# Optimization experiments

Hardware: AMD Instinct MI355X
Metric: run time of the kernel (lower is better)

The kernel has to match this reference:

```python
import jax, jax.numpy as jnp
import numpy as np

D = 1024
LEAF_DIM = 512
DEPTH = 3
NUM_LEAVES = 2 ** DEPTH          # 8
NUM_NODES = NUM_LEAVES - 1       # 7
B, T = 4, 2048


def setup_inputs() -> dict:
    key = jax.random.key(0)
    ks = jax.random.split(key, 9)
    sD = 1.0 / np.sqrt(D)
    sH = 1.0 / np.sqrt(LEAF_DIM)
    return {
        "x": jax.random.normal(ks[0], (B, T, D), dtype=jnp.float32),
        "node_kernel": jax.random.normal(ks[1], (D, NUM_NODES), dtype=jnp.float32) * sD,
        "node_bias": jnp.zeros((NUM_NODES,), dtype=jnp.float32),
        "w1a": jax.random.normal(ks[2], (NUM_LEAVES, D, LEAF_DIM), dtype=jnp.float32) * sD,
        "w1b": jax.random.normal(ks[3], (NUM_LEAVES, D, LEAF_DIM), dtype=jnp.float32) * sD,
        "b1a": jnp.zeros((NUM_LEAVES, LEAF_DIM), dtype=jnp.float32),
        "b1b": jnp.zeros((NUM_LEAVES, LEAF_DIM), dtype=jnp.float32),
        "w2": jax.random.normal(ks[4], (NUM_LEAVES, LEAF_DIM, D), dtype=jnp.float32) * sH,
        "b2": jnp.zeros((NUM_LEAVES, D), dtype=jnp.float32),
    }


def reference(x, node_kernel, node_bias, w1a, w1b, b1a, b1b, w2, b2):
    Bx, Tx, Dx = x.shape
    L = NUM_LEAVES
    # hierarchical sigmoid gates over tree nodes: (B,T,num_nodes)
    c = jax.nn.sigmoid(jnp.einsum("btd,dn->btn", x, node_kernel) + node_bias)
    # interleave [c_i, 1-c_i] -> (B,T,2*num_nodes,1), matching original stack+reshape
    c_nc = jnp.stack([c, 1.0 - c], axis=-1).reshape(Bx, Tx, -1)[..., None]
    # build per-leaf mixture weights by descending the tree (depth is a small constant)
    mixture = jnp.ones((Bx, Tx, L), dtype=x.dtype)
    for d in range(DEPTH):
        n2 = 2 ** (d + 1)  # 2 * n_nodes at this level
        mixture = mixture.reshape(Bx, Tx, n2, L // n2) * c_nc[..., :n2, :]
    mixture = mixture.reshape(Bx, Tx, L)
    # per-leaf GLU MLP, batched over the leaf axis
    h = (jnp.einsum("btd,ldh->btlh", x, w1a) + b1a) * (
        jnp.einsum("btd,ldh->btlh", x, w1b) + b1b
    )  # (B,T,L,leaf_dim)
    y = jnp.einsum("btlh,lhd->btld", h, w2) + b2  # (B,T,L,D)
    # weighted combine over leaves
    return (y * mixture[..., None]).sum(axis=-2)  # (B,T,D)
```

## Files before the change

kernel.cpp:

```cpp
#include <hip/hip_runtime.h>


typedef unsigned short u16;
typedef __attribute__((ext_vector_type(8))) short bf16x8;
typedef __attribute__((ext_vector_type(8))) unsigned short u16x8;
typedef __attribute__((ext_vector_type(4))) float f32x4;

__device__ __forceinline__ u16 f2bf(float f) {
  unsigned int u = __builtin_bit_cast(unsigned int, f);
  u += 0x7FFFu + ((u >> 16) & 1u);
  return (u16)(u >> 16);
}

__device__ __forceinline__ void gload16(const void* g, void* l) {
  __builtin_amdgcn_global_load_lds(
      (const __attribute__((address_space(1))) unsigned int*)g,
      (__attribute__((address_space(3))) unsigned int*)l, 16, 0, 0);
}

__device__ __forceinline__ f32x4 MFMA(bf16x8 a, bf16x8 b, f32x4 c) {
  return __builtin_amdgcn_mfma_f32_16x16x32_bf16(a, b, c, 0, 0, 0);
}

#define BARX()                              \
  do {                                      \
    __builtin_amdgcn_sched_barrier(0);      \
    __builtin_amdgcn_s_barrier();           \
    __builtin_amdgcn_sched_barrier(0);      \
  } while (0)

#define VMC(n)                                             \
  do {                                                     \
    __builtin_amdgcn_sched_barrier(0);                     \
    asm volatile("s_waitcnt vmcnt(" #n ")" ::: "memory");  \
    __builtin_amdgcn_sched_barrier(0);                     \
  } while (0)

__global__ void k_gate(const float* __restrict__ x, const float* __restrict__ nk,
                       const float* __restrict__ nb, float* __restrict__ mix) {
  int token = blockIdx.x * 4 + (threadIdx.x >> 6);
  int lane = threadIdx.x & 63;
  const float* xr = x + (size_t)token * 1024;
  float a0 = 0.f, a1 = 0.f, a2 = 0.f, a3 = 0.f;
#pragma unroll
  for (int j = 0; j < 16; ++j) {
    int d = lane + j * 64;
    float xv = xr[d];
    const float* nkd = nk + d * 7;
    a0 = fmaf(xv, nkd[0], a0);
    a1 = fmaf(xv, nkd[1], a1);
    a2 = fmaf(xv, nkd[2], a2);
    a3 = fmaf(xv, nkd[3], a3);
  }
#pragma unroll
  for (int off = 32; off >= 1; off >>= 1) {
    a0 += __shfl_xor(a0, off);
    a1 += __shfl_xor(a1, off);
    a2 += __shfl_xor(a2, off);
    a3 += __shfl_xor(a3, off);
  }
  if (lane == 0) {
    float v[4] = {a0 + nb[0], a1 + nb[1], a2 + nb[2], a3 + nb[3]};
    float cn[8];
#pragma unroll
    for (int i = 0; i < 4; ++i) {
      float s = 1.f / (1.f + expf(-v[i]));
      cn[2 * i] = s;
      cn[2 * i + 1] = 1.f - s;
    }
    float* mr = mix + (size_t)token * 8;
#pragma unroll
    for (int l = 0; l < 8; ++l) mr[l] = cn[l >> 2] * cn[l >> 1] * cn[l];
  }
}

__global__ void k_cast_x(const float* __restrict__ x, u16* __restrict__ xb) {
  size_t i = (size_t)blockIdx.x * blockDim.x + threadIdx.x;
  const float4* p = (const float4*)x + i * 2;
  float4 v0 = p[0], v1 = p[1];
  u16x8 o;
  o[0] = f2bf(v0.x); o[1] = f2bf(v0.y); o[2] = f2bf(v0.z); o[3] = f2bf(v0.w);
  o[4] = f2bf(v1.x); o[5] = f2bf(v1.y); o[6] = f2bf(v1.z); o[7] = f2bf(v1.w);
  *((u16x8*)xb + i) = o;
}

__global__ void k_transpose_cast(const float* __restrict__ in, u16* __restrict__ out,
                                 int R, int C, long out_rstride, long leaf_base) {
  __shared__ float tile[32][33];
  int l = blockIdx.z;
  int c0 = blockIdx.x * 32, r0 = blockIdx.y * 32;
  const float* inl = in + (size_t)l * R * C;
  int tc = threadIdx.x & 31, tr = threadIdx.x >> 5;
#pragma unroll
  for (int i = 0; i < 4; ++i) {
    int r = tr + i * 8;
    tile[r][tc] = inl[(size_t)(r0 + r) * C + c0 + tc];
  }
  __syncthreads();
  u16* outl = out + (size_t)l * leaf_base;
#pragma unroll
  for (int i = 0; i < 4; ++i) {
    int c = tr + i * 8;
    outl[(size_t)(c0 + c) * out_rstride + r0 + tc] = f2bf(tile[tc][c]);
  }
}

__global__ __launch_bounds__(256, 2) void k_glu_gemm(
    const u16* __restrict__ Xb, const u16* __restrict__ Wa, const u16* __restrict__ Wb,
    const float* __restrict__ b1a, const float* __restrict__ b1b,
    const float* __restrict__ mix, u16* __restrict__ H) {
  constexpr int K = 1024, NT = 32;
  __shared__ alignas(16) u16 smem[24576];
  const int tid = threadIdx.x;
  const int logical = (blockIdx.x & 7) * 256 + (blockIdx.x >> 3);
  const int bn = logical >> 6, bm = logical & 63;
  const int m0 = bm * 128, n0 = bn * 128;
  const int wid = tid >> 6, lane = tid & 63;
  const int wm = (wid >> 1) * 64, wn = (wid & 1) * 64;
  const int fr = lane & 15, fk = lane >> 4;

  const int c0_ = tid, c1_ = tid + 256;
  const int r0_ = c0_ >> 2, s0_ = ((c0_ & 3) ^ ((r0_ >> 1) & 3)) * 8;
  const int r1_ = c1_ >> 2, s1_ = ((c1_ & 3) ^ ((r1_ >> 1) & 3)) * 8;

#define STG1(v)                                                                     \
  do {                                                                              \
    const int kb = (v) * 32;                                                        \
    u16* dA = smem + ((v) & 1) * 4096;                                              \
    u16* dBa = smem + 8192 + ((v) & 1) * 4096;                                      \
    u16* dBb = smem + 16384 + ((v) & 1) * 4096;                                     \
    gload16(&Xb[(size_t)(m0 + r0_) * K + kb + s0_], &dA[c0_ * 8]);                  \
    gload16(&Xb[(size_t)(m0 + r1_) * K + kb + s1_], &dA[c1_ * 8]);                  \
    gload16(&Wa[(size_t)(n0 + r0_) * K + kb + s0_], &dBa[c0_ * 8]);                 \
    gload16(&Wa[(size_t)(n0 + r1_) * K + kb + s1_], &dBa[c1_ * 8]);                 \
    gload16(&Wb[(size_t)(n0 + r0_) * K + kb + s0_], &dBb[c0_ * 8]);                 \
    gload16(&Wb[(size_t)(n0 + r1_) * K + kb + s1_], &dBb[c1_ * 8]);                 \
  } while (0)

  f32x4 accA[4][4], accB[4][4];
#pragma unroll
  for (int i = 0; i < 4; ++i)
#pragma unroll
    for (int j = 0; j < 4; ++j) {
      accA[i][j] = (f32x4)0.0f;
      accB[i][j] = (f32x4)0.0f;
    }

  const int slot_ = (fk ^ ((fr >> 1) & 3)) * 8;

  STG1(0);
  VMC(0);
  BARX();
  for (int u = 0; u < NT; ++u) {
    if (u + 1 < NT) STG1(u + 1);
    __builtin_amdgcn_sched_barrier(0);
    const u16* A_ = smem + (u & 1) * 4096;
    const u16* Ba_ = smem + 8192 + (u & 1) * 4096;
    const u16* Bb_ = smem + 16384 + (u & 1) * 4096;
    bf16x8 a_[4], ba_[4], bb_[4];
#pragma unroll
    for (int i = 0; i < 4; ++i) {
      a_[i]  = *(const bf16x8*)&A_[(wm + i * 16 + fr) * 32 + slot_];
      ba_[i] = *(const bf16x8*)&Ba_[(wn + i * 16 + fr) * 32 + slot_];
      bb_[i] = *(const bf16x8*)&Bb_[(wn + i * 16 + fr) * 32 + slot_];
    }
    __builtin_amdgcn_s_setprio(1);
#pragma unroll
    for (int i = 0; i < 4; ++i)
#pragma unroll
      for (int j = 0; j < 4; ++j) {
        accA[i][j] = MFMA(a_[i], ba_[j], accA[i][j]);
        accB[i][j] = MFMA(a_[i], bb_[j], accB[i][j]);
      }
    __builtin_amdgcn_s_setprio(0);
    VMC(0);
    BARX();
  }
#undef STG1

  const int leaf = n0 >> 9;
  const float* b1al = b1a + (leaf << 9);
  const float* b1bl = b1b + (leaf << 9);
  u16* hs = smem;
#pragma unroll
  for (int mf = 0; mf < 4; ++mf)
#pragma unroll
    for (int r = 0; r < 4; ++r) {
      int row_l = wm + mf * 16 + fk * 4 + r;
      float mv = mix[(size_t)(m0 + row_l) * 8 + leaf];
#pragma unroll
      for (int nf = 0; nf < 4; ++nf) {
        int col_l = wn + nf * 16 + fr;
        int hc = (n0 + col_l) & 511;
        float va = accA[mf][nf][r] + b1al[hc];
        float vb = accB[mf][nf][r] + b1bl[hc];
        hs[row_l * 128 + col_l] = f2bf(va * vb * mv);
      }
    }
  BARX();
#pragma unroll
  for (int j = 0; j < 8; ++j) {
    int idx = j * 256 + tid;
    int row_l = idx >> 4;
    int cc = (idx & 15) * 8;
    *(u16x8*)&H[(size_t)(m0 + row_l) * 4096 + n0 + cc] =
        *(const u16x8*)&hs[row_l * 128 + cc];
  }
}

__global__ __launch_bounds__(256, 4) void k_gemm2s(
    const u16* __restrict__ Hm, const u16* __restrict__ W2T,
    const float* __restrict__ b2, const float* __restrict__ mix,
    float* __restrict__ out, float* __restrict__ P1) {
  constexpr int K = 4096, KH = 2048, NT = KH / 32;
  __shared__ alignas(16) u16 smem[16384];
  const int tid = threadIdx.x;
  const int logical = (blockIdx.x & 7) * 128 + (blockIdx.x >> 3);
  const int xcd_chunk = logical >> 7;
  const int i_ = logical & 127;
  const int kc = i_ >> 6;
  const int bn = i_ & 7;
  const int bm = xcd_chunk * 8 + ((i_ >> 3) & 7);
  const int m0 = bm * 128, n0 = bn * 128;
  const size_t kbase = (size_t)kc * KH;
  const int wid = tid >> 6, lane = tid & 63;
  const int wm = (wid >> 1) * 64, wn = (wid & 1) * 64;
  const int fr = lane & 15, fk = lane >> 4;

  const int c0_ = tid, c1_ = tid + 256;
  const int r0_ = c0_ >> 2, s0_ = ((c0_ & 3) ^ ((r0_ >> 1) & 3)) * 8;
  const int r1_ = c1_ >> 2, s1_ = ((c1_ & 3) ^ ((r1_ >> 1) & 3)) * 8;

#define STG2(v)                                                                       \
  do {                                                                                \
    const int kb = (v) * 32;                                                          \
    u16* dA = smem + ((v) & 1) * 4096;                                                \
    u16* dB = smem + 8192 + ((v) & 1) * 4096;                                         \
    gload16(&Hm[(size_t)(m0 + r0_) * K + kbase + kb + s0_], &dA[c0_ * 8]);            \
    gload16(&Hm[(size_t)(m0 + r1_) * K + kbase + kb + s1_], &dA[c1_ * 8]);            \
    gload16(&W2T[(size_t)(n0 + r0_) * K + kbase + kb + s0_], &dB[c0_ * 8]);           \
    gload16(&W2T[(size_t)(n0 + r1_) * K + kbase + kb + s1_], &dB[c1_ * 8]);           \
  } while (0)

  f32x4 acc[4][4];
#pragma unroll
  for (int i = 0; i < 4; ++i)
#pragma unroll
    for (int j = 0; j < 4; ++j) acc[i][j] = (f32x4)0.0f;

  const int slot_ = (fk ^ ((fr >> 1) & 3)) * 8;

  STG2(0);
  VMC(0);
  BARX();
  for (int u = 0; u < NT; ++u) {
    if (u + 1 < NT) STG2(u + 1);
    __builtin_amdgcn_sched_barrier(0);
    const u16* A_ = smem + (u & 1) * 4096;
    const u16* B_ = smem + 8192 + (u & 1) * 4096;
    bf16x8 a_[4], b_[4];
#pragma unroll
    for (int i = 0; i < 4; ++i) {
      a_[i] = *(const bf16x8*)&A_[(wm + i * 16 + fr) * 32 + slot_];
      b_[i] = *(const bf16x8*)&B_[(wn + i * 16 + fr) * 32 + slot_];
    }
    __builtin_amdgcn_s_setprio(1);
#pragma unroll
    for (int i = 0; i < 4; ++i)
#pragma unroll
      for (int j = 0; j < 4; ++j)
        acc[i][j] = MFMA(a_[i], b_[j], acc[i][j]);
    __builtin_amdgcn_s_setprio(0);
    VMC(0);
    BARX();
  }
#undef STG2

  float* dst = (kc == 0) ? out : P1;
  float* os = (float*)smem;
  const int myhalf = wid >> 1;
#pragma unroll
  for (int half = 0; half < 2; ++half) {
    BARX();
    if (myhalf == half) {
#pragma unroll
      for (int nf = 0; nf < 4; ++nf) {
        int col_l = wn + nf * 16 + fr;
        float bc[8];
        if (kc == 0) {
#pragma unroll
          for (int l = 0; l < 8; ++l) bc[l] = b2[l * 1024 + n0 + col_l];
        }
#pragma unroll
        for (int mf = 0; mf < 4; ++mf)
#pragma unroll
          for (int r = 0; r < 4; ++r) {
            int row_lh = mf * 16 + fk * 4 + r;
            float v = acc[mf][nf][r];
            if (kc == 0) {
              const float* mr = mix + (size_t)(m0 + half * 64 + row_lh) * 8;
              float bias = 0.f;
#pragma unroll
              for (int l = 0; l < 8; ++l) bias = fmaf(mr[l], bc[l], bias);
              v += bias;
            }
            os[row_lh * 128 + col_l] = v;
          }
      }
    }
    BARX();
#pragma unroll
    for (int j = 0; j < 8; ++j) {
      int idx = j * 256 + tid;
      int row_lh = idx >> 5;
      int cc = (idx & 31) * 4;
      *(float4*)&dst[(size_t)(m0 + half * 64 + row_lh) * 1024 + n0 + cc] =
          *(const float4*)&os[row_lh * 128 + cc];
    }
  }
}

__global__ void k_add(float* __restrict__ out, const float* __restrict__ P1) {
  size_t i = (size_t)blockIdx.x * 256 + threadIdx.x;
  float4 a = ((const float4*)out)[i];
  float4 b = ((const float4*)P1)[i];
  a.x += b.x; a.y += b.y; a.z += b.z; a.w += b.w;
  ((float4*)out)[i] = a;
}

extern "C" void kernel_launch(void* const* d_in, const int* in_sizes, int n_in,
                              void* d_out, int out_size, void* d_ws, size_t ws_size,
                              hipStream_t stream) {
  const float* x   = (const float*)d_in[0];
  const float* nk  = (const float*)d_in[1];
  const float* nb  = (const float*)d_in[2];
  const float* w1a = (const float*)d_in[3];
  const float* w1b = (const float*)d_in[4];
  const float* b1a = (const float*)d_in[5];
  const float* b1b = (const float*)d_in[6];
  const float* w2  = (const float*)d_in[7];
  const float* b2  = (const float*)d_in[8];
  float* out = (float*)d_out;

  char* ws = (char*)d_ws;
  float* mix = (float*)ws;
  u16* Xb  = (u16*)(ws + 262144);
  u16* WaT = (u16*)(ws + 262144 + 16777216);
  u16* WbT = (u16*)(ws + 262144 + 16777216 + 8388608);
  u16* W2T = (u16*)(ws + 262144 + 16777216 + 2 * 8388608);
  u16* Hs  = (u16*)(ws + 262144 + 16777216 + 3 * 8388608);
  float* P1 = (float*)(ws + 262144);

  k_gate<<<2048, 256, 0, stream>>>(x, nk, nb, mix);
  k_cast_x<<<4096, 256, 0, stream>>>(x, Xb);
  k_transpose_cast<<<dim3(16, 32, 8), 256, 0, stream>>>(w1a, WaT, 1024, 512, 1024L, 512L * 1024L);
  k_transpose_cast<<<dim3(16, 32, 8), 256, 0, stream>>>(w1b, WbT, 1024, 512, 1024L, 512L * 1024L);
  k_transpose_cast<<<dim3(32, 16, 8), 256, 0, stream>>>(w2, W2T, 512, 1024, 4096L, 512L);
  k_glu_gemm<<<2048, 256, 0, stream>>>(Xb, WaT, WbT, b1a, b1b, mix, Hs);
  k_gemm2s<<<1024, 256, 0, stream>>>(Hs, W2T, b2, mix, out, P1);
  k_add<<<8192, 256, 0, stream>>>(out, P1);
}
```

Baseline: 285.4 us.

## Fuse gate with x cast, merge w1 transposes, remap GLU tile order

Merges the gating kernel and the x-to-bf16 cast into one kernel, so x is read once and two launches become one. The two w1a/w1b transpose-cast launches are combined into a single grid. The GLU GEMM block-to-tile mapping is changed so each XCD chunk works on a group of 4 N-tiles across all M-tiles, which is meant to improve L2 reuse of weights. The gate kernel now reads node_kernel with a strided per-lane pattern, which may coalesce less well.

```diff
diff --git a/kernel.cpp b/kernel.cpp
--- a/kernel.cpp
+++ b/kernel.cpp
@@ -36,21 +36,31 @@
     __builtin_amdgcn_sched_barrier(0);                     \
   } while (0)
 
-__global__ void k_gate(const float* __restrict__ x, const float* __restrict__ nk,
-                       const float* __restrict__ nb, float* __restrict__ mix) {
+__global__ void k_gatecast(const float* __restrict__ x, const float* __restrict__ nk,
+                           const float* __restrict__ nb, float* __restrict__ mix,
+                           u16* __restrict__ xb) {
   int token = blockIdx.x * 4 + (threadIdx.x >> 6);
   int lane = threadIdx.x & 63;
   const float* xr = x + (size_t)token * 1024;
+  u16* xbr = xb + (size_t)token * 1024;
   float a0 = 0.f, a1 = 0.f, a2 = 0.f, a3 = 0.f;
 #pragma unroll
-  for (int j = 0; j < 16; ++j) {
-    int d = lane + j * 64;
-    float xv = xr[d];
-    const float* nkd = nk + d * 7;
-    a0 = fmaf(xv, nkd[0], a0);
-    a1 = fmaf(xv, nkd[1], a1);
-    a2 = fmaf(xv, nkd[2], a2);
-    a3 = fmaf(xv, nkd[3], a3);
+  for (int j = 0; j < 2; ++j) {
+    int base = j * 512 + lane * 8;
+    float4 p0 = *(const float4*)&xr[base];
+    float4 p1 = *(const float4*)&xr[base + 4];
+    float v[8] = {p0.x, p0.y, p0.z, p0.w, p1.x, p1.y, p1.z, p1.w};
+    u16x8 o;
+#pragma unroll
+    for (int t = 0; t < 8; ++t) {
+      const float* nkd = nk + (size_t)(base + t) * 7;
+      a0 = fmaf(v[t], nkd[0], a0);
+      a1 = fmaf(v[t], nkd[1], a1);
+      a2 = fmaf(v[t], nkd[2], a2);
+      a3 = fmaf(v[t], nkd[3], a3);
+      o[t] = f2bf(v[t]);
+    }
+    *(u16x8*)&xbr[base] = o;
   }
 #pragma unroll
   for (int off = 32; off >= 1; off >>= 1) {
@@ -60,11 +70,11 @@
     a3 += __shfl_xor(a3, off);
   }
   if (lane == 0) {
-    float v[4] = {a0 + nb[0], a1 + nb[1], a2 + nb[2], a3 + nb[3]};
+    float v4[4] = {a0 + nb[0], a1 + nb[1], a2 + nb[2], a3 + nb[3]};
     float cn[8];
 #pragma unroll
     for (int i = 0; i < 4; ++i) {
-      float s = 1.f / (1.f + expf(-v[i]));
+      float s = 1.f / (1.f + expf(-v4[i]));
       cn[2 * i] = s;
       cn[2 * i + 1] = 1.f - s;
     }
@@ -72,16 +82,6 @@
 #pragma unroll
     for (int l = 0; l < 8; ++l) mr[l] = cn[l >> 2] * cn[l >> 1] * cn[l];
   }
-}
-
-__global__ void k_cast_x(const float* __restrict__ x, u16* __restrict__ xb) {
-  size_t i = (size_t)blockIdx.x * blockDim.x + threadIdx.x;
-  const float4* p = (const float4*)x + i * 2;
-  float4 v0 = p[0], v1 = p[1];
-  u16x8 o;
-  o[0] = f2bf(v0.x); o[1] = f2bf(v0.y); o[2] = f2bf(v0.z); o[3] = f2bf(v0.w);
-  o[4] = f2bf(v1.x); o[5] = f2bf(v1.y); o[6] = f2bf(v1.z); o[7] = f2bf(v1.w);
-  *((u16x8*)xb + i) = o;
 }
 
 __global__ void k_transpose_cast(const float* __restrict__ in, u16* __restrict__ out,
@@ -102,6 +102,30 @@
   for (int i = 0; i < 4; ++i) {
     int c = tr + i * 8;
     outl[(size_t)(c0 + c) * out_rstride + r0 + tc] = f2bf(tile[tc][c]);
+  }
+}
+
+__global__ void k_transpose_w1(const float* __restrict__ w1a, const float* __restrict__ w1b,
+                               u16* __restrict__ WaT, u16* __restrict__ WbT) {
+  __shared__ float tile[32][33];
+  int z = blockIdx.z;
+  int l = z & 7;
+  const float* in = (z < 8) ? w1a : w1b;
+  u16* out = (z < 8) ? WaT : WbT;
+  int c0 = blockIdx.x * 32, r0 = blockIdx.y * 32;
+  const float* inl = in + (size_t)l * 1024 * 512;
+  int tc = threadIdx.x & 31, tr = threadIdx.x >> 5;
+#pragma unroll
+  for (int i = 0; i < 4; ++i) {
+    int r = tr + i * 8;
+    tile[r][tc] = inl[(size_t)(r0 + r) * 512 + c0 + tc];
+  }
+  __syncthreads();
+  u16* outl = out + (size_t)l * 512 * 1024;
+#pragma unroll
+  for (int i = 0; i < 4; ++i) {
+    int c = tr + i * 8;
+    outl[(size_t)(c0 + c) * 1024 + r0 + tc] = f2bf(tile[tc][c]);
   }
 }
 
@@ -113,7 +137,10 @@
   __shared__ alignas(16) u16 smem[24576];
   const int tid = threadIdx.x;
   const int logical = (blockIdx.x & 7) * 256 + (blockIdx.x >> 3);
-  const int bn = logical >> 6, bm = logical & 63;
+  const int xcd_chunk = logical >> 8;
+  const int i_ = logical & 255;
+  const int bn = xcd_chunk * 4 + (i_ & 3);
+  const int bm = i_ >> 2;
   const int m0 = bm * 128, n0 = bn * 128;
   const int wid = tid >> 6, lane = tid & 63;
   const int wm = (wid >> 1) * 64, wn = (wid & 1) * 64;
@@ -351,10 +378,8 @@
   u16* Hs  = (u16*)(ws + 262144 + 16777216 + 3 * 8388608);
   float* P1 = (float*)(ws + 262144);
 
-  k_gate<<<2048, 256, 0, stream>>>(x, nk, nb, mix);
-  k_cast_x<<<4096, 256, 0, stream>>>(x, Xb);
-  k_transpose_cast<<<dim3(16, 32, 8), 256, 0, stream>>>(w1a, WaT, 1024, 512, 1024L, 512L * 1024L);
-  k_transpose_cast<<<dim3(16, 32, 8), 256, 0, stream>>>(w1b, WbT, 1024, 512, 1024L, 512L * 1024L);
+  k_gatecast<<<2048, 256, 0, stream>>>(x, nk, nb, mix, Xb);
+  k_transpose_w1<<<dim3(16, 32, 16), 256, 0, stream>>>(w1a, w1b, WaT, WbT);
   k_transpose_cast<<<dim3(32, 16, 8), 256, 0, stream>>>(w2, W2T, 512, 1024, 4096L, 512L);
   k_glu_gemm<<<2048, 256, 0, stream>>>(Xb, WaT, WbT, b1a, b1b, mix, Hs);
   k_gemm2s<<<1024, 256, 0, stream>>>(Hs, W2T, b2, mix, out, P1);
```

Result: faster. 275.7 us (-3.4%).
